# Kernel optimization log

Measured on AMD Instinct MI355X. Metric: run time of the kernel, lower is better.

The kernel has to match this reference:

```python
import jax, jax.numpy as jnp
import numpy as np

N_NODES = 8192
N_EDGES = 65536
D_MODEL = 64
D_INNER = 128
D_STATE = 16
DT_RANK = 4
LAYER_NUM = 3
TAU = 0.01


def _unif(key, shape, fan_out):
    stdv = 1.0 / np.sqrt(fan_out)
    return jax.random.uniform(key, shape, jnp.float32, -stdv, stdv)


def setup_inputs() -> dict:
    key = jax.random.key(0)
    ks = jax.random.split(key, 12)
    x = jax.random.normal(ks[0], (N_NODES, D_MODEL), jnp.float32)
    edge_index = jax.random.randint(ks[1], (2, N_EDGES), 0, N_NODES, jnp.int64)
    in_proj_w = _unif(ks[2], (D_MODEL, 2 * D_INNER), 2 * D_INNER)
    x_proj_w = _unif(ks[3], (D_INNER, DT_RANK + 2 * D_STATE), DT_RANK + 2 * D_STATE)
    dt_proj_w = _unif(ks[4], (DT_RANK, D_INNER), D_INNER)
    out_proj_w = _unif(ks[5], (D_INNER, D_MODEL), D_MODEL)
    A_log = jnp.log(jnp.broadcast_to(jnp.arange(1, D_STATE + 1, dtype=jnp.float32)[None, :], (D_INNER, D_STATE)))
    D = jnp.ones((D_INNER,), jnp.float32)
    in_act_w = _unif(ks[6], (D_INNER, 2), 2)
    in_act_b = _unif(ks[7], (2,), 2)
    out_act_w = _unif(ks[8], (D_INNER, 2), 2)
    out_act_b = _unif(ks[9], (2,), 2)
    return {"x": x, "in_proj_w": in_proj_w, "x_proj_w": x_proj_w, "dt_proj_w": dt_proj_w,
            "A_log": A_log, "D": D, "out_proj_w": out_proj_w,
            "in_act_w": in_act_w, "in_act_b": in_act_b, "out_act_w": out_act_w, "out_act_b": out_act_b,
            "edge_index": edge_index, "layer_num": LAYER_NUM}


def _norm_adj(row, col, w, n_nodes):
    # SparseTensor(...).set_diag() adds diag value 1; symmetric deg^-1/2 renorm
    deg = jax.ops.segment_sum(w, row, num_segments=n_nodes) + 1.0
    dinv = jnp.where(deg > 0, deg ** -0.5, 0.0)
    return dinv[row] * w * dinv[col], dinv * dinv  # off-diag edge weights, diag weights


def _spmm(row, col, ew, dw, x, n_nodes):
    # adj @ x with adj = edges(ew) + diag(dw); x: [N, F]
    return jax.ops.segment_sum(ew[:, None] * x[col], row, num_segments=n_nodes) + dw[:, None] * x


def _gumbel_hard(logits, key, tau):
    g = jax.random.gumbel(key, logits.shape, logits.dtype)
    y = jax.nn.softmax((logits + g) / tau, axis=-1)
    hard = jax.nn.one_hot(jnp.argmax(y, axis=-1), logits.shape[-1], dtype=y.dtype)
    return hard + y - jax.lax.stop_gradient(y)


def reference(x, in_proj_w, x_proj_w, dt_proj_w, A_log, D, out_proj_w,
              in_act_w, in_act_b, out_act_w, out_act_b, edge_index, layer_num):
    n_nodes, d_model = x.shape
    d_inner = dt_proj_w.shape[1]
    n = A_log.shape[1]
    dt_rank = dt_proj_w.shape[0]
    row, col = edge_index[0], edge_index[1]

    xl = jnp.broadcast_to(x[:, None, :], (n_nodes, layer_num, d_model))  # [N,L,d_model]
    x_and_res = xl @ in_proj_w                                           # [N,L,2*d_inner]
    xs, res = jnp.split(x_and_res, 2, axis=-1)
    xs = jax.nn.relu(xs)                                                 # u in scan

    A = -jnp.exp(A_log)                                                  # [d_inner, n]
    x_dbl = xs @ x_proj_w                                                # [N,L,dt_rank+2n]
    delta = jax.nn.softplus(x_dbl[..., :dt_rank] @ dt_proj_w)            # [N,L,d_inner]
    B = x_dbl[..., dt_rank:dt_rank + n]                                  # [N,L,n]
    C = x_dbl[..., dt_rank + n:]                                         # [N,L,n]

    deltaA = jnp.exp(jnp.einsum('bld,dn->bldn', delta, A))               # [N,L,d_inner,n]
    deltaB_u = jnp.einsum('bld,bln->bldn', delta * xs, B)                # [N,L,d_inner,n]

    # initial adjacency: unit-weight edges, sym-normalized with self loops
    ew, dw = _norm_adj(row, col, jnp.ones((row.shape[0],), xs.dtype), n_nodes)
    state = jnp.zeros((n_nodes, d_inner, n), xs.dtype)
    gkey = jax.random.key(42)
    ys = []
    for i in range(layer_num):  # small fixed number of GCN/SSM steps
        state = deltaA[:, i] * state + deltaB_u[:, i]
        y = jnp.einsum('bdn,bn->bd', state, C[:, i])                     # [N,d_inner]
        flat = _spmm(row, col, ew, dw, state.reshape(n_nodes, d_inner * n), n_nodes)
        state = flat.reshape(n_nodes, d_inner, n)
        in_p = _gumbel_hard(y @ in_act_w + in_act_b, jax.random.fold_in(gkey, 2 * i), TAU)
        out_p = _gumbel_hard(y @ out_act_w + out_act_b, jax.random.fold_in(gkey, 2 * i + 1), TAU)
        w = in_p[col, 0] * out_p[row, 0]  # keep_in_prob[v] * keep_out_prob[u]
        ew, dw = _norm_adj(row, col, w, n_nodes)
        ys.append(y)

    y = jnp.stack(ys, axis=1) + xs * D                                   # [N,L,d_inner]
    y = y * jax.nn.relu(res)
    out = y @ out_proj_w                                                 # [N,L,d_model]
    return out[:, -1, :]
```

## Files before the change

kernel.cpp:

```cpp
#include <hip/hip_runtime.h>
#include <cstdint>

#define NN 8192
#define NE 65536
#define G 16
#define CAP 64

typedef _Float16 h4 __attribute__((ext_vector_type(4)));
typedef _Float16 h2 __attribute__((ext_vector_type(2)));

__host__ __device__ inline void tf2x32(uint32_t k0, uint32_t k1,
                                       uint32_t x0, uint32_t x1,
                                       uint32_t& r0, uint32_t& r1) {
  uint32_t ks2 = k0 ^ k1 ^ 0x1BD11BDAu;
  x0 += k0; x1 += k1;
#define TF_ROT(x,d) (((x)<<(d))|((x)>>(32-(d))))
#define TF_R4(ra,rb,rc,rd) \
  x0+=x1; x1=TF_ROT(x1,ra); x1^=x0; \
  x0+=x1; x1=TF_ROT(x1,rb); x1^=x0; \
  x0+=x1; x1=TF_ROT(x1,rc); x1^=x0; \
  x0+=x1; x1=TF_ROT(x1,rd); x1^=x0;
  TF_R4(13,15,26,6)  x0+=k1;  x1+=ks2+1u;
  TF_R4(17,29,16,24) x0+=ks2; x1+=k0+2u;
  TF_R4(13,15,26,6)  x0+=k0;  x1+=k1+3u;
  TF_R4(17,29,16,24) x0+=k1;  x1+=ks2+4u;
  TF_R4(13,15,26,6)  x0+=ks2; x1+=k0+5u;
  r0=x0; r1=x1;
#undef TF_R4
#undef TF_ROT
}

__device__ inline float gumbel32(uint32_t k0, uint32_t k1, uint32_t idx) {
  uint32_t a, b;
  tf2x32(k0, k1, 0u, idx, a, b);
  uint32_t bits = a ^ b;
  float f = __uint_as_float((bits >> 9) | 0x3f800000u) - 1.0f;
  float u = (f > 0.0f) ? f : 1.17549435e-38f;
  return -logf(-logf(u));
}

__global__ void k_zero(int* __restrict__ p, int n) {
  int i = blockIdx.x*blockDim.x + threadIdx.x;
  if (i < n) p[i] = 0;
}

__global__ void k_scatter(const int* __restrict__ ei, int* __restrict__ cnt,
                          int* __restrict__ csr_col) {
  int e = blockIdx.x*blockDim.x + threadIdx.x;
  if (e < NE) {
    int v = ei[e];
    int pos = atomicAdd(&cnt[v], 1);
    if (pos < CAP) csr_col[(v<<6) + pos] = ei[NE + e];
  }
}

__global__ __launch_bounds__(256) void k_nodeprep(
    const float* __restrict__ x, const float* __restrict__ ipw,
    const float* __restrict__ xpw, const float* __restrict__ dtw,
    const float* __restrict__ iaw, const float* __restrict__ iab,
    const float* __restrict__ oaw, const float* __restrict__ oab,
    const float* __restrict__ alog,
    uint32_t ki0, uint32_t ki1, uint32_t ko0, uint32_t ko1,
    float* __restrict__ xs, float* __restrict__ rres,
    float* __restrict__ delta, _Float16* __restrict__ dxh2,
    float* __restrict__ Bm, _Float16* __restrict__ Bh,
    float* __restrict__ Cm,
    float* __restrict__ inp, float* __restrict__ outp,
    float* __restrict__ Amat) {
  __shared__ float sx[G][64];
  __shared__ float sxs[G][128];
  __shared__ float sdbl[G][36];
  __shared__ float sdx[2][128];
  __shared__ float4 sred4[4];
  int t = threadIdx.x;
  int b0 = blockIdx.x * G;
  if (blockIdx.x == 0) {
    for (int i = t; i < 2048; i += 256) Amat[i] = -expf(alog[i]);
  }
  for (int i = t; i < G*64; i += 256) sx[i>>6][i&63] = x[b0*64 + i];
  __syncthreads();
  float acc[G];
#pragma unroll
  for (int g = 0; g < G; g++) acc[g] = 0.f;
  for (int k = 0; k < 64; k++) {
    float w = ipw[k*256 + t];
#pragma unroll
    for (int g = 0; g < G; g++) acc[g] += sx[g][k] * w;
  }
  if (t < 128) {
#pragma unroll
    for (int g = 0; g < G; g++) {
      float v = fmaxf(acc[g], 0.f);
      sxs[g][t] = v;
      xs[(size_t)(b0+g)*128 + t] = v;
    }
  } else {
    int j = t - 128;
#pragma unroll
    for (int g = 0; g < G; g++) rres[(size_t)(b0+g)*128 + j] = fmaxf(acc[g], 0.f);
  }
  __syncthreads();
  for (int idx = t; idx < G*36; idx += 256) {
    int g = idx / 36, c = idx % 36;
    float a = 0.f;
    for (int d = 0; d < 128; d++) a += sxs[g][d] * xpw[d*36 + c];
    sdbl[g][c] = a;
    if (c >= 4 && c < 20) {
      Bm[(b0+g)*16 + (c-4)] = a;
      Bh[(b0+g)*16 + (c-4)] = (_Float16)a;
    } else if (c >= 20)    Cm[(b0+g)*16 + (c-20)] = a;
  }
  __syncthreads();
  int d = t & 127;
  int hi = t >> 7;
  int lane = t & 63, wv = t >> 6;
  for (int gg = 0; gg < G/2; gg++) {
    int g = hi*(G/2) + gg;
    int b = b0 + g;
    float dt = sdbl[g][0]*dtw[d]     + sdbl[g][1]*dtw[128+d]
             + sdbl[g][2]*dtw[256+d] + sdbl[g][3]*dtw[384+d];
    float dv = fmaxf(dt, 0.f) + log1pf(expf(-fabsf(dt)));
    delta[(size_t)b*128 + d] = dv;
    float dxv = dv * sxs[g][d];
    sdx[hi][d] = dxv;
    float4 pr;
    pr.x = dxv * iaw[2*d];   pr.y = dxv * iaw[2*d+1];
    pr.z = dxv * oaw[2*d];   pr.w = dxv * oaw[2*d+1];
    for (int off = 32; off >= 1; off >>= 1) {
      pr.x += __shfl_down(pr.x, off);
      pr.y += __shfl_down(pr.y, off);
      pr.z += __shfl_down(pr.z, off);
      pr.w += __shfl_down(pr.w, off);
    }
    if (lane == 0) sred4[wv] = pr;
    __syncthreads();
    if (d < 64) {
      h2 pk;
      pk.x = (_Float16)sdx[hi][d];
      pk.y = (_Float16)sdx[hi][d + 64];
      ((h2*)(dxh2 + ((size_t)b << 7)))[d] = pk;
    }
    if (d == 0) {
      float4 q0 = sred4[hi*2], q1 = sred4[hi*2 + 1];
      float BC = 0.f;
      for (int n = 0; n < 16; n++) BC += sdbl[g][4+n] * sdbl[g][20+n];
      float li0 = BC*(q0.x+q1.x) + iab[0], li1 = BC*(q0.y+q1.y) + iab[1];
      float lo0 = BC*(q0.z+q1.z) + oab[0], lo1 = BC*(q0.w+q1.w) + oab[1];
      uint32_t L0 = 2u*(uint32_t)b, L1 = L0 + 1u;
      inp[b]  = (li0 + gumbel32(ki0, ki1, L0) >= li1 + gumbel32(ki0, ki1, L1)) ? 1.0f : 0.0f;
      outp[b] = (lo0 + gumbel32(ko0, ko1, L0) >= lo1 + gumbel32(ko0, ko1, L1)) ? 1.0f : 0.0f;
    }
    __syncthreads();
  }
}

__global__ __launch_bounds__(256) void k_spmm0f(
    const int* __restrict__ cnt, const int* __restrict__ csr_col,
    const float* __restrict__ inp, const float* __restrict__ outp,
    const float* __restrict__ delta, const _Float16* __restrict__ dxh2,
    const float* __restrict__ Bm, const _Float16* __restrict__ Bh,
    const float* __restrict__ Cm, const float* __restrict__ Amat,
    _Float16* __restrict__ s_out, float* __restrict__ dinv1,
    float* __restrict__ y2p) {
  __shared__ int   sc[CAP];
  __shared__ float scoef[CAP];
  __shared__ float sgate[CAP];
  __shared__ float sdegs;
  int v = blockIdx.x, t = threadIdx.x;
  int deg = min(cnt[v], CAP);
  if (t < deg) {
    int c = csr_col[(v<<6) + t];
    sc[t] = c;
    scoef[t] = 1.0f / sqrtf((float)min(cnt[c], CAP) + 1.0f);
    sgate[t] = inp[c];
  }
  __syncthreads();
  if (t < 64) {
    float g = (t < deg) ? sgate[t] : 0.f;
    for (int off = 32; off >= 1; off >>= 1) g += __shfl_down(g, off);
    if (t == 0) sdegs = g;
  }
  int d0 = t >> 2, d1 = d0 + 64, nb = t & 3;
  float dv = 1.0f / sqrtf((float)deg + 1.0f);
  float4 Bv = ((const float4*)(Bm + ((size_t)v << 4)))[nb];
  h2 pkv = ((const h2*)(dxh2 + ((size_t)v << 7)))[d0];
  float dx0 = (float)pkv.x, dx1 = (float)pkv.y;
  float dw = dv * dv;
  float c0 = dw * dx0, c1 = dw * dx1;
  float4 a0 = {c0*Bv.x, c0*Bv.y, c0*Bv.z, c0*Bv.w};
  float4 a1 = {c1*Bv.x, c1*Bv.y, c1*Bv.z, c1*Bv.w};
  for (int j = 0; j < deg; j++) {
    int c = sc[j];
    float coef = dv * scoef[j];
    h2 pk = ((const h2*)(dxh2 + ((size_t)c << 7)))[d0];
    h4 Bp = ((const h4*)(Bh + ((size_t)c << 4)))[nb];
    float e0 = coef * (float)pk.x;
    float e1 = coef * (float)pk.y;
    float bx = (float)Bp.x, by = (float)Bp.y, bz = (float)Bp.z, bw = (float)Bp.w;
    a0.x += e0*bx; a0.y += e0*by; a0.z += e0*bz; a0.w += e0*bw;
    a1.x += e1*bx; a1.y += e1*by; a1.z += e1*bz; a1.w += e1*bw;
  }
  float de0 = delta[v*128 + d0], de1 = delta[v*128 + d1];
  float4 A0 = ((const float4*)(Amat + (d0 << 4)))[nb];
  float4 A1 = ((const float4*)(Amat + (d1 << 4)))[nb];
  float4 E0, E1;
  E0.x = expf(de0*A0.x); E0.y = expf(de0*A0.y); E0.z = expf(de0*A0.z); E0.w = expf(de0*A0.w);
  E1.x = expf(de1*A1.x); E1.y = expf(de1*A1.y); E1.z = expf(de1*A1.z); E1.w = expf(de1*A1.w);
  float4 s0, s1;
  s0.x = E0.x*a0.x + dx0*Bv.x;  s0.y = E0.y*a0.y + dx0*Bv.y;
  s0.z = E0.z*a0.z + dx0*Bv.z;  s0.w = E0.w*a0.w + dx0*Bv.w;
  s1.x = E1.x*a1.x + dx1*Bv.x;  s1.y = E1.y*a1.y + dx1*Bv.y;
  s1.z = E1.z*a1.z + dx1*Bv.z;  s1.w = E1.w*a1.w + dx1*Bv.w;
  if (inp[v] != 0.f) {
    h4* op = (h4*)(s_out + ((size_t)v << 11));
    h4 h0, h1;
    h0.x = (_Float16)s0.x; h0.y = (_Float16)s0.y; h0.z = (_Float16)s0.z; h0.w = (_Float16)s0.w;
    h1.x = (_Float16)s1.x; h1.y = (_Float16)s1.y; h1.z = (_Float16)s1.z; h1.w = (_Float16)s1.w;
    op[t] = h0; op[t + 256] = h1;
  }
  __syncthreads();
  float degs = sdegs;
  float d1v = 1.0f / sqrtf(outp[v]*degs + 1.0f);
  if (t == 0) dinv1[v] = d1v;
  float dw1 = d1v * d1v;
  float4 Cv = ((const float4*)(Cm + ((size_t)v << 4)))[nb];
  float y0p = dw1*(E0.x*s0.x*Cv.x + E0.y*s0.y*Cv.y + E0.z*s0.z*Cv.z + E0.w*s0.w*Cv.w)
            + dx0*(Bv.x*Cv.x + Bv.y*Cv.y + Bv.z*Cv.z + Bv.w*Cv.w);
  float y1p = dw1*(E1.x*s1.x*Cv.x + E1.y*s1.y*Cv.y + E1.z*s1.z*Cv.z + E1.w*s1.w*Cv.w)
            + dx1*(Bv.x*Cv.x + Bv.y*Cv.y + Bv.z*Cv.z + Bv.w*Cv.w);
  y0p += __shfl_xor(y0p, 1); y0p += __shfl_xor(y0p, 2);
  y1p += __shfl_xor(y1p, 1); y1p += __shfl_xor(y1p, 2);
  if (nb == 0) {
    y2p[v*128 + d0] = y0p;
    y2p[v*128 + d1] = y1p;
  }
}

__global__ __launch_bounds__(256) void k_spmm1fo(
    const int* __restrict__ cnt, const int* __restrict__ csr_col,
    const float* __restrict__ dinv1,
    const float* __restrict__ inp, const float* __restrict__ outp,
    const float* __restrict__ delta,
    const float* __restrict__ Cm, const float* __restrict__ Amat,
    const _Float16* __restrict__ s_in, const float* __restrict__ y2p,
    const float* __restrict__ xs, const float* __restrict__ rres,
    const float* __restrict__ Dv, const float* __restrict__ wout,
    float* __restrict__ out) {
  __shared__ int   sc[CAP];
  __shared__ float scoef[CAP];
  __shared__ int   snact;
  __shared__ float ty[128];
  int v = blockIdx.x, t = threadIdx.x;
  if (t == 0) snact = 0;
  __syncthreads();
  int deg = (outp[v] != 0.f) ? min(cnt[v], CAP) : 0;
  if (t < deg) {
    int c = csr_col[(v<<6) + t];
    if (inp[c] != 0.f) {
      int p = atomicAdd(&snact, 1);
      sc[p] = c; scoef[p] = dinv1[c];
    }
  }
  __syncthreads();
  int nact = snact;
  int d0 = t >> 2, d1 = d0 + 64, nb = t & 3;
  float dv = dinv1[v];
  float4 a0 = {0.f,0.f,0.f,0.f}, a1 = {0.f,0.f,0.f,0.f};
  for (int j = 0; j < nact; j++) {
    int c = sc[j];
    float coef = dv * scoef[j];
    const h4* nbp = (const h4*)(s_in + ((size_t)c << 11));
    h4 n0 = nbp[t], n1 = nbp[t + 256];
    a0.x += coef*(float)n0.x; a0.y += coef*(float)n0.y;
    a0.z += coef*(float)n0.z; a0.w += coef*(float)n0.w;
    a1.x += coef*(float)n1.x; a1.y += coef*(float)n1.y;
    a1.z += coef*(float)n1.z; a1.w += coef*(float)n1.w;
  }
  float y0g = 0.f, y1g = 0.f;
  if (nact > 0) {
    float de0 = delta[v*128 + d0], de1 = delta[v*128 + d1];
    float4 A0 = ((const float4*)(Amat + (d0 << 4)))[nb];
    float4 A1 = ((const float4*)(Amat + (d1 << 4)))[nb];
    float4 Cv = ((const float4*)(Cm + ((size_t)v << 4)))[nb];
    y0g = expf(de0*A0.x)*a0.x*Cv.x + expf(de0*A0.y)*a0.y*Cv.y +
          expf(de0*A0.z)*a0.z*Cv.z + expf(de0*A0.w)*a0.w*Cv.w;
    y1g = expf(de1*A1.x)*a1.x*Cv.x + expf(de1*A1.y)*a1.y*Cv.y +
          expf(de1*A1.z)*a1.z*Cv.z + expf(de1*A1.w)*a1.w*Cv.w;
  }
  y0g += __shfl_xor(y0g, 1); y0g += __shfl_xor(y0g, 2);
  y1g += __shfl_xor(y1g, 1); y1g += __shfl_xor(y1g, 2);
  if (nb == 0) {
    float yA = y0g + y2p[v*128 + d0];
    float yB = y1g + y2p[v*128 + d1];
    ty[d0] = (yA + xs[v*128 + d0]*Dv[d0]) * rres[v*128 + d0];
    ty[d1] = (yB + xs[v*128 + d1]*Dv[d1]) * rres[v*128 + d1];
  }
  __syncthreads();
  if (t < 64) {
    float acc = 0.f;
    for (int d = 0; d < 128; d++) acc += ty[d] * wout[d*64 + t];
    out[v*64 + t] = acc;
  }
}

extern "C" void kernel_launch(void* const* d_in, const int* in_sizes, int n_in,
                              void* d_out, int out_size, void* d_ws, size_t ws_size,
                              hipStream_t stream) {
  const float* x    = (const float*)d_in[0];
  const float* ipw  = (const float*)d_in[1];
  const float* xpw  = (const float*)d_in[2];
  const float* dtw  = (const float*)d_in[3];
  const float* alog = (const float*)d_in[4];
  const float* Dv   = (const float*)d_in[5];
  const float* wout = (const float*)d_in[6];
  const float* iaw  = (const float*)d_in[7];
  const float* iab  = (const float*)d_in[8];
  const float* oaw  = (const float*)d_in[9];
  const float* oab  = (const float*)d_in[10];
  const int*   ei   = (const int*)d_in[11];
  (void)in_sizes; (void)n_in; (void)out_size; (void)ws_size;

  float* W = (float*)d_ws;
  size_t o = 0;
  float* xs    = W + o; o += (size_t)NN*128;
  float* rres  = W + o; o += (size_t)NN*128;
  float* delta = W + o; o += (size_t)NN*128;
  float* y2p   = W + o; o += (size_t)NN*128;
  float* Bm    = W + o; o += (size_t)NN*16;
  float* Cm    = W + o; o += (size_t)NN*16;
  float* Amat  = W + o; o += 2048;
  float* dinv1 = W + o; o += NN;
  float* inp   = W + o; o += NN;
  float* outp  = W + o; o += NN;
  _Float16* dxh2 = (_Float16*)(W + o); o += (size_t)NN*64;
  _Float16* Bh   = (_Float16*)(W + o); o += (size_t)NN*8;
  _Float16* stA  = (_Float16*)(W + o); o += (size_t)NN*1024;
  int* cnt     = (int*)(W + o);
  int* csr_col = cnt + NN;

  uint32_t ki0, ki1, ko0, ko1;
  tf2x32(0u, 42u, 0u, 0u, ki0, ki1);
  tf2x32(0u, 42u, 0u, 1u, ko0, ko1);

  k_zero<<<NN/256, 256, 0, stream>>>(cnt, NN);
  k_scatter<<<NE/256, 256, 0, stream>>>(ei, cnt, csr_col);

  k_nodeprep<<<NN/G, 256, 0, stream>>>(x, ipw, xpw, dtw, iaw, iab, oaw, oab,
                                       alog, ki0, ki1, ko0, ko1,
                                       xs, rres, delta, dxh2, Bm, Bh, Cm,
                                       inp, outp, Amat);

  k_spmm0f<<<NN, 256, 0, stream>>>(cnt, csr_col, inp, outp,
                                   delta, dxh2, Bm, Bh, Cm, Amat,
                                   stA, dinv1, y2p);

  k_spmm1fo<<<NN, 256, 0, stream>>>(cnt, csr_col, dinv1, inp, outp,
                                    delta, Cm, Amat, stA, y2p,
                                    xs, rres, Dv, wout, (float*)d_out);
}
```

Measured before the change: 181.3 us.

## Halve nodes per block and restructure gate reductions to one wave per node

Node-prep now handles 8 nodes per block instead of 16, which doubles the block count for better occupancy across CUs. The per-node loop with two __syncthreads per iteration is replaced by a single pass that computes delta and dx for all nodes into shared memory. Each wave then does a complete 128-wide gate reduction for two nodes, so the cross-wave shared-memory combine goes away. This cuts barriers and serialization, but the per-block setup work, including the x_proj matvec loads, is amortized over fewer nodes.

```diff
diff --git a/kernel.cpp b/kernel.cpp
--- a/kernel.cpp
+++ b/kernel.cpp
@@ -3,7 +3,7 @@
 
 #define NN 8192
 #define NE 65536
-#define G 16
+#define G 8
 #define CAP 64
 
 typedef _Float16 h4 __attribute__((ext_vector_type(4)));
@@ -70,8 +70,7 @@
   __shared__ float sx[G][64];
   __shared__ float sxs[G][128];
   __shared__ float sdbl[G][36];
-  __shared__ float sdx[2][128];
-  __shared__ float4 sred4[4];
+  __shared__ float sdx[G][128];
   int t = threadIdx.x;
   int b0 = blockIdx.x * G;
   if (blockIdx.x == 0) {
@@ -111,46 +110,53 @@
     } else if (c >= 20)    Cm[(b0+g)*16 + (c-20)] = a;
   }
   __syncthreads();
-  int d = t & 127;
-  int hi = t >> 7;
-  int lane = t & 63, wv = t >> 6;
-  for (int gg = 0; gg < G/2; gg++) {
-    int g = hi*(G/2) + gg;
+  {
+    int d = t & 127, hi = t >> 7;
+#pragma unroll
+    for (int gg = 0; gg < G/2; gg++) {
+      int g = hi*(G/2) + gg;
+      int b = b0 + g;
+      float dt = sdbl[g][0]*dtw[d]     + sdbl[g][1]*dtw[128+d]
+               + sdbl[g][2]*dtw[256+d] + sdbl[g][3]*dtw[384+d];
+      float dv = fmaxf(dt, 0.f) + log1pf(expf(-fabsf(dt)));
+      delta[(size_t)b*128 + d] = dv;
+      sdx[g][d] = dv * sxs[g][d];
+    }
+  }
+  __syncthreads();
+  for (int i = t; i < G*64; i += 256) {
+    int g = i >> 6, d = i & 63;
+    h2 pk;
+    pk.x = (_Float16)sdx[g][d];
+    pk.y = (_Float16)sdx[g][d + 64];
+    ((h2*)(dxh2 + ((size_t)(b0+g) << 7)))[d] = pk;
+  }
+  int wid = t >> 6, lane = t & 63;
+#pragma unroll
+  for (int s = 0; s < 2; s++) {
+    int g = wid*2 + s;
     int b = b0 + g;
-    float dt = sdbl[g][0]*dtw[d]     + sdbl[g][1]*dtw[128+d]
-             + sdbl[g][2]*dtw[256+d] + sdbl[g][3]*dtw[384+d];
-    float dv = fmaxf(dt, 0.f) + log1pf(expf(-fabsf(dt)));
-    delta[(size_t)b*128 + d] = dv;
-    float dxv = dv * sxs[g][d];
-    sdx[hi][d] = dxv;
+    float da = sdx[g][lane], db = sdx[g][lane + 64];
     float4 pr;
-    pr.x = dxv * iaw[2*d];   pr.y = dxv * iaw[2*d+1];
-    pr.z = dxv * oaw[2*d];   pr.w = dxv * oaw[2*d+1];
+    pr.x = da*iaw[2*lane]   + db*iaw[2*(lane+64)];
+    pr.y = da*iaw[2*lane+1] + db*iaw[2*(lane+64)+1];
+    pr.z = da*oaw[2*lane]   + db*oaw[2*(lane+64)];
+    pr.w = da*oaw[2*lane+1] + db*oaw[2*(lane+64)+1];
     for (int off = 32; off >= 1; off >>= 1) {
       pr.x += __shfl_down(pr.x, off);
       pr.y += __shfl_down(pr.y, off);
       pr.z += __shfl_down(pr.z, off);
       pr.w += __shfl_down(pr.w, off);
     }
-    if (lane == 0) sred4[wv] = pr;
-    __syncthreads();
-    if (d < 64) {
-      h2 pk;
-      pk.x = (_Float16)sdx[hi][d];
-      pk.y = (_Float16)sdx[hi][d + 64];
-      ((h2*)(dxh2 + ((size_t)b << 7)))[d] = pk;
-    }
-    if (d == 0) {
-      float4 q0 = sred4[hi*2], q1 = sred4[hi*2 + 1];
+    if (lane == 0) {
       float BC = 0.f;
       for (int n = 0; n < 16; n++) BC += sdbl[g][4+n] * sdbl[g][20+n];
-      float li0 = BC*(q0.x+q1.x) + iab[0], li1 = BC*(q0.y+q1.y) + iab[1];
-      float lo0 = BC*(q0.z+q1.z) + oab[0], lo1 = BC*(q0.w+q1.w) + oab[1];
+      float li0 = BC*pr.x + iab[0], li1 = BC*pr.y + iab[1];
+      float lo0 = BC*pr.z + oab[0], lo1 = BC*pr.w + oab[1];
       uint32_t L0 = 2u*(uint32_t)b, L1 = L0 + 1u;
       inp[b]  = (li0 + gumbel32(ki0, ki1, L0) >= li1 + gumbel32(ki0, ki1, L1)) ? 1.0f : 0.0f;
       outp[b] = (lo0 + gumbel32(ko0, ko1, L0) >= lo1 + gumbel32(ko0, ko1, L1)) ? 1.0f : 0.0f;
     }
-    __syncthreads();
   }
 }
 
```

New measurement: 168.7 us. 7.0% less time.
